# Optimization experiments

Hardware: AMD Instinct MI355X
Metric: run time of the kernel (lower is better)

The kernel has to match this reference:

```python
import jax, jax.numpy as jnp
import numpy as np

N = 32768       # flattened residues (batch*seq)
DIM = 1024      # dim == channel (required by residual add)
NRES = 21       # amino-acid types
RECYCLES = 2


def _quat_to_rot(q):
    w, x, y, z = q[..., 0], q[..., 1], q[..., 2], q[..., 3]
    return jnp.stack([
        jnp.stack([1 - 2 * (y * y + z * z), 2 * (x * y - w * z), 2 * (x * z + w * y)], -1),
        jnp.stack([2 * (x * y + w * z), 1 - 2 * (x * x + z * z), 2 * (y * z - w * x)], -1),
        jnp.stack([2 * (x * z - w * y), 2 * (y * z + w * x), 1 - 2 * (x * x + y * y)], -1),
    ], -2)


def _rand_rigid(key, shape, tscale=1.0):
    # random valid rigid transforms as 4x4 homogeneous matrices
    kq, kt = jax.random.split(key)
    q = jax.random.normal(kq, shape + (4,), jnp.float32)
    q = q / jnp.linalg.norm(q, axis=-1, keepdims=True)
    rot = _quat_to_rot(q)
    t = jax.random.normal(kt, shape + (3,), jnp.float32) * tscale
    m = jnp.zeros(shape + (4, 4), jnp.float32)
    m = m.at[..., :3, :3].set(rot).at[..., :3, 3].set(t).at[..., 3, 3].set(1.0)
    return m


def setup_inputs():
    key = jax.random.key(0)
    ks = jax.random.split(key, 12)
    s = 1.0 / np.sqrt(DIM)
    return {
        "rep0": jax.random.normal(ks[0], (N, DIM), jnp.float32),
        "rep1": jax.random.normal(ks[1], (N, DIM), jnp.float32),
        "w_in": jax.random.normal(ks[2], (DIM, DIM), jnp.float32) * s,
        "b_in": jnp.zeros((DIM,), jnp.float32),
        "w1": jax.random.normal(ks[3], (DIM, DIM), jnp.float32) * s,
        "b1": jnp.zeros((DIM,), jnp.float32),
        "w2": jax.random.normal(ks[4], (DIM, DIM), jnp.float32) * s,
        "b2": jnp.zeros((DIM,), jnp.float32),
        "w_ang": jax.random.normal(ks[5], (DIM, 14), jnp.float32) * s,
        "b_ang": jnp.zeros((14,), jnp.float32),
        "rigids": _rand_rigid(ks[6], (N,), tscale=10.0),              # backbone frames
        "default_frames": _rand_rigid(ks[7], (NRES, 8), tscale=1.5), # restype_rigid_group_default_frame
        "lit_positions": jax.random.normal(ks[8], (NRES, 14, 3), jnp.float32),
        "atom_mask": (jax.random.uniform(ks[9], (NRES, 14)) > 0.2).astype(jnp.float32),
        "aatype": jax.random.randint(ks[10], (N,), 0, NRES),
        "group_idx": jax.random.randint(ks[11], (NRES, 14), 0, 8),   # restype_atom14_to_rigid_group
    }


def reference(rep0, rep1, w_in, b_in, w1, b1, w2, b2, w_ang, b_ang,
              rigids, default_frames, lit_positions, atom_mask, aatype, group_idx):
    # InputProjection: shared ReLU+Linear applied to each representation, summed
    act = (jax.nn.relu(rep0) @ w_in + b_in) + (jax.nn.relu(rep1) @ w_in + b_in)
    # ResidueBlock with residual recycles: act += Linear(ReLU(Linear(ReLU(act))))
    for _ in range(RECYCLES):
        h = jax.nn.relu(act) @ w1 + b1
        h = jax.nn.relu(h) @ w2 + b2
        act = act + h
    # TorisonAngles: Linear(dim,14) -> (N,7,2) -> l2_normalize
    ang = (jax.nn.relu(act) @ w_ang + b_ang).reshape(N, 7, 2)
    angles = ang / jnp.sqrt(jnp.maximum(jnp.sum(ang * ang, -1, keepdims=True), 1e-12))
    # torsion_angles_to_frames: prepend identity backbone angle (sin=0, cos=1)
    sin = jnp.concatenate([jnp.zeros((N, 1), angles.dtype), angles[..., 0]], 1)  # [N,8]
    cos = jnp.concatenate([jnp.ones((N, 1), angles.dtype), angles[..., 1]], 1)
    z = jnp.zeros_like(sin); one = jnp.ones_like(sin)
    rotx = jnp.stack([
        jnp.stack([one, z, z, z], -1),
        jnp.stack([z, cos, -sin, z], -1),
        jnp.stack([z, sin, cos, z], -1),
        jnp.stack([z, z, z, one], -1),
    ], -2)                                            # [N,8,4,4] rotation about x by torsion
    frames = default_frames[aatype] @ rotx            # [N,8,4,4]
    # chi2/chi3/chi4 frames are defined relative to the previous chi frame
    f5 = frames[:, 4] @ frames[:, 5]
    f6 = f5 @ frames[:, 6]
    f7 = f6 @ frames[:, 7]
    frames_to_bb = jnp.concatenate([frames[:, :5], jnp.stack([f5, f6, f7], 1)], 1)
    frames_global = rigids[:, None] @ frames_to_bb    # [N,8,4,4]
    # frames_and_literature_positions_to_atom14_pos
    gidx = group_idx[aatype]                          # [N,14] rigid-group id per atom
    f14 = jnp.take_along_axis(frames_global,
                              jnp.broadcast_to(gidx[:, :, None, None], (N, 14, 4, 4)),
                              axis=1)                 # [N,14,4,4]
    pos = lit_positions[aatype]                       # [N,14,3]
    pred = jnp.einsum('naij,naj->nai', f14[..., :3, :3], pos) + f14[..., :3, 3]
    pred = pred * atom_mask[aatype][..., None]        # [N,14,3]
    return angles, pred, frames_global
```

## Files before the change

### kernel.cpp

```cpp
#include <hip/hip_runtime.h>
#include <stdint.h>

typedef uint16_t u16;
typedef uint32_t u32;
typedef __bf16 bf16;
typedef bf16 bf16x8 __attribute__((ext_vector_type(8)));
typedef float f32x4 __attribute__((ext_vector_type(4)));

#define N_RES 32768
#define DIM 1024

__device__ __forceinline__ float b2f(u16 u) {
  u32 v = ((u32)u) << 16;
  float f;
  __builtin_memcpy(&f, &v, 4);
  return f;
}
__device__ __forceinline__ u16 f2b(float f) {
  u32 u;
  __builtin_memcpy(&u, &f, 4);
  u += 0x7fffu + ((u >> 16) & 1u);
  return (u16)(u >> 16);
}
__device__ __forceinline__ void split2(float v, u16& h, u16& l) {
  h = f2b(v);
  l = f2b(v - b2f(h));
}
__device__ __forceinline__ void relu_mask4(uint4& h, uint4& l) {
  u32 s, m;
  s = h.x & 0x80008000u; m = ((s >> 15) & 0x00010001u) * 0xFFFFu; h.x &= ~m; l.x &= ~m;
  s = h.y & 0x80008000u; m = ((s >> 15) & 0x00010001u) * 0xFFFFu; h.y &= ~m; l.y &= ~m;
  s = h.z & 0x80008000u; m = ((s >> 15) & 0x00010001u) * 0xFFFFu; h.z &= ~m; l.z &= ~m;
  s = h.w & 0x80008000u; m = ((s >> 15) & 0x00010001u) * 0xFFFFu; h.w &= ~m; l.w &= ~m;
}
__device__ __forceinline__ void relu_split8(bf16x8& h, bf16x8& l) {
  uint4 uh, ul;
  __builtin_memcpy(&uh, &h, 16);
  __builtin_memcpy(&ul, &l, 16);
  relu_mask4(uh, ul);
  __builtin_memcpy(&h, &uh, 16);
  __builtin_memcpy(&l, &ul, 16);
}
__device__ __forceinline__ void split8(const float* v, uint4& H, uint4& L) {
  u16 h[8], l[8];
#pragma unroll
  for (int i = 0; i < 8; ++i) split2(v[i], h[i], l[i]);
  H.x = (u32)h[0] | ((u32)h[1] << 16);
  H.y = (u32)h[2] | ((u32)h[3] << 16);
  H.z = (u32)h[4] | ((u32)h[5] << 16);
  H.w = (u32)h[6] | ((u32)h[7] << 16);
  L.x = (u32)l[0] | ((u32)l[1] << 16);
  L.y = (u32)l[2] | ((u32)l[3] << 16);
  L.z = (u32)l[4] | ((u32)l[5] << 16);
  L.w = (u32)l[6] | ((u32)l[7] << 16);
}

__device__ __forceinline__ void g2l16(const void* g, void* lds) {
  __builtin_amdgcn_global_load_lds(
      (__attribute__((address_space(1))) void*)(g),
      (__attribute__((address_space(3))) void*)(lds), 16, 0, 0);
}

__global__ __launch_bounds__(256) void transpose_split(const float* __restrict__ in,
                                                       u16* __restrict__ outh,
                                                       u16* __restrict__ outl) {
  __shared__ float t[32][33];
  const int bx = blockIdx.x * 32, by = blockIdx.y * 32;
  const int tx = threadIdx.x, ty = threadIdx.y;
  for (int i = ty; i < 32; i += 8) t[i][tx] = in[(size_t)(by + i) * DIM + bx + tx];
  __syncthreads();
  for (int i = ty; i < 32; i += 8) {
    u16 h, l;
    split2(t[tx][i], h, l);
    const size_t o = (size_t)(bx + i) * DIM + by + tx;
    outh[o] = h;
    outl[o] = l;
  }
}

__global__ __launch_bounds__(256) void prep_input(const float* __restrict__ rep0,
                                                  const float* __restrict__ rep1,
                                                  u16* __restrict__ oh,
                                                  u16* __restrict__ ol) {
  const size_t base = ((size_t)blockIdx.x * 256 + threadIdx.x) * 8;
  float4 x0 = *(const float4*)(rep0 + base);
  float4 x1 = *(const float4*)(rep0 + base + 4);
  float4 y0 = *(const float4*)(rep1 + base);
  float4 y1 = *(const float4*)(rep1 + base + 4);
  float v[8];
  v[0] = fmaxf(x0.x, 0.f) + fmaxf(y0.x, 0.f);
  v[1] = fmaxf(x0.y, 0.f) + fmaxf(y0.y, 0.f);
  v[2] = fmaxf(x0.z, 0.f) + fmaxf(y0.z, 0.f);
  v[3] = fmaxf(x0.w, 0.f) + fmaxf(y0.w, 0.f);
  v[4] = fmaxf(x1.x, 0.f) + fmaxf(y1.x, 0.f);
  v[5] = fmaxf(x1.y, 0.f) + fmaxf(y1.y, 0.f);
  v[6] = fmaxf(x1.z, 0.f) + fmaxf(y1.z, 0.f);
  v[7] = fmaxf(x1.w, 0.f) + fmaxf(y1.w, 0.f);
  uint4 H, L;
  split8(v, H, L);
  *(uint4*)(oh + base) = H;
  *(uint4*)(ol + base) = L;
}

__global__ __launch_bounds__(256, 3) void gemm_split(
    const u16* __restrict__ Ah, const u16* __restrict__ Al, int reluA,
    const u16* __restrict__ Bh, const u16* __restrict__ Bl,
    const float* __restrict__ bias, float bscale,
    const u16* __restrict__ Rh, const u16* __restrict__ Rl,
    u16* __restrict__ Oh, u16* __restrict__ Ol) {
  __shared__ __align__(16) u32 SMEM[6144];
  u16* AS = (u16*)SMEM;
  u16* BS = (u16*)SMEM + 8192;
  u32* C_lds = SMEM;

  const int tid = threadIdx.x;
  const int wave = tid >> 6;
  const int lane = tid & 63;
  const int lrow = lane & 15;
  const int lquad = lane >> 4;

  const int g = blockIdx.x + (blockIdx.y << 4);
  const int xcd = g & 7;
  const int j = g >> 3;
  const int bm = (xcd * 32 + (j >> 4)) * 128;
  const int bn = (j & 15) * 64;

  const int wm = (wave & 1) * 64;
  const int wn = (wave >> 1) * 32;

  f32x4 acc[4][2];
#pragma unroll
  for (int i = 0; i < 4; ++i)
#pragma unroll
    for (int jj = 0; jj < 2; ++jj) acc[i][jj] = (f32x4){0.f, 0.f, 0.f, 0.f};

  const int srow = tid >> 3;
  const int dc = (tid & 7) ^ (srow & 7);
  const size_t scol = (size_t)(dc & 3) * 8;
  const u16* srcA = ((dc < 4) ? Ah : Al) + (size_t)(bm + srow) * DIM + scol;
  const u16* srcB = ((dc < 4) ? Bh : Bl) + (size_t)(bn + srow) * DIM + scol;
  u16* dA = AS + (size_t)tid * 8;
  u16* dB = BS + (size_t)tid * 8;

  const int swzH = ((lquad ^ (lrow & 7)) * 8);
  const int swzL = swzH ^ 32;

  for (int kt = 0; kt < 32; ++kt) {
    const size_t ko = (size_t)kt * 32;
#pragma unroll
    for (int is = 0; is < 4; ++is)
      g2l16(srcA + ko + (size_t)is * 32 * DIM, dA + is * 2048);
#pragma unroll
    for (int is = 0; is < 2; ++is)
      g2l16(srcB + ko + (size_t)is * 32 * DIM, dB + is * 2048);
    __syncthreads();

    bf16x8 a_h[4], a_l[4], b_h[2], b_l[2];
#pragma unroll
    for (int i = 0; i < 4; ++i) {
      const u16* arow = AS + (wm + i * 16 + lrow) * 64;
      a_h[i] = *(const bf16x8*)(arow + swzH);
      a_l[i] = *(const bf16x8*)(arow + swzL);
      if (reluA) relu_split8(a_h[i], a_l[i]);
    }
#pragma unroll
    for (int jj = 0; jj < 2; ++jj) {
      const u16* brow = BS + (wn + jj * 16 + lrow) * 64;
      b_h[jj] = *(const bf16x8*)(brow + swzH);
      b_l[jj] = *(const bf16x8*)(brow + swzL);
    }
#pragma unroll
    for (int i = 0; i < 4; ++i)
#pragma unroll
      for (int jj = 0; jj < 2; ++jj) {
        acc[i][jj] = __builtin_amdgcn_mfma_f32_16x16x32_bf16(a_h[i], b_h[jj], acc[i][jj], 0, 0, 0);
        acc[i][jj] = __builtin_amdgcn_mfma_f32_16x16x32_bf16(a_h[i], b_l[jj], acc[i][jj], 0, 0, 0);
        acc[i][jj] = __builtin_amdgcn_mfma_f32_16x16x32_bf16(a_l[i], b_h[jj], acc[i][jj], 0, 0, 0);
      }
    __syncthreads();
  }

#pragma unroll
  for (int half = 0; half < 2; ++half) {
    if (wm == half * 64) {
#pragma unroll
      for (int jj = 0; jj < 2; ++jj) {
        const int colL = wn + jj * 16 + lrow;
        const float bj = bias[bn + colL] * bscale;
#pragma unroll
        for (int i = 0; i < 4; ++i) {
#pragma unroll
          for (int r = 0; r < 4; ++r) {
            const int row = i * 16 + lquad * 4 + r;
            u16 h, l;
            split2(acc[i][jj][r] + bj, h, l);
            C_lds[row * 64 + (colL ^ ((row & 7) << 2))] = (u32)h | ((u32)l << 16);
          }
        }
      }
    }
    __syncthreads();
    {
      const int wv = tid >> 6;
      const int lr8 = (lane >> 3);
      const int cg = lane & 7;
#pragma unroll
      for (int g2 = 0; g2 < 2; ++g2) {
        const int row = wv * 16 + g2 * 8 + lr8;
        const int swz = (row & 7) << 2;
        const u32* crow = C_lds + row * 64;
        const int cb = cg * 8;
        uint4 qa = *(const uint4*)&crow[cb ^ swz];
        uint4 qb = *(const uint4*)&crow[(cb + 4) ^ swz];
        float v[8];
        v[0] = b2f((u16)(qa.x & 0xFFFF)) + b2f((u16)(qa.x >> 16));
        v[1] = b2f((u16)(qa.y & 0xFFFF)) + b2f((u16)(qa.y >> 16));
        v[2] = b2f((u16)(qa.z & 0xFFFF)) + b2f((u16)(qa.z >> 16));
        v[3] = b2f((u16)(qa.w & 0xFFFF)) + b2f((u16)(qa.w >> 16));
        v[4] = b2f((u16)(qb.x & 0xFFFF)) + b2f((u16)(qb.x >> 16));
        v[5] = b2f((u16)(qb.y & 0xFFFF)) + b2f((u16)(qb.y >> 16));
        v[6] = b2f((u16)(qb.z & 0xFFFF)) + b2f((u16)(qb.z >> 16));
        v[7] = b2f((u16)(qb.w & 0xFFFF)) + b2f((u16)(qb.w >> 16));
        const int grow = bm + half * 64 + row;
        const size_t gbase = (size_t)grow * DIM + bn + cb;
        if (Rh) {
          uint4 rh = *(const uint4*)(Rh + gbase);
          uint4 rl = *(const uint4*)(Rl + gbase);
          v[0] += b2f((u16)(rh.x & 0xFFFF)) + b2f((u16)(rl.x & 0xFFFF));
          v[1] += b2f((u16)(rh.x >> 16)) + b2f((u16)(rl.x >> 16));
          v[2] += b2f((u16)(rh.y & 0xFFFF)) + b2f((u16)(rl.y & 0xFFFF));
          v[3] += b2f((u16)(rh.y >> 16)) + b2f((u16)(rl.y >> 16));
          v[4] += b2f((u16)(rh.z & 0xFFFF)) + b2f((u16)(rl.z & 0xFFFF));
          v[5] += b2f((u16)(rh.z >> 16)) + b2f((u16)(rl.z >> 16));
          v[6] += b2f((u16)(rh.w & 0xFFFF)) + b2f((u16)(rl.w & 0xFFFF));
          v[7] += b2f((u16)(rh.w >> 16)) + b2f((u16)(rl.w >> 16));
        }
        uint4 H, L;
        split8(v, H, L);
        *(uint4*)(Oh + gbase) = H;
        *(uint4*)(Ol + gbase) = L;
      }
    }
    __syncthreads();
  }
}

__global__ __launch_bounds__(256) void angles_split(
    const u16* __restrict__ ACTh, const u16* __restrict__ ACTl,
    const u16* __restrict__ WAh, const u16* __restrict__ WAl,
    const float* __restrict__ b_ang, float* __restrict__ out_angles) {
  const int tid = threadIdx.x;
  const int wave = tid >> 6, lane = tid & 63;
  const int lrow = lane & 15, lquad = lane >> 4;
  const int rowA = blockIdx.x * 64 + wave * 16 + lrow;
  f32x4 acc = (f32x4){0.f, 0.f, 0.f, 0.f};
  const u16* gah = ACTh + (size_t)rowA * DIM + lquad * 8;
  const u16* gal = ACTl + (size_t)rowA * DIM + lquad * 8;
  const u16* gbh = WAh + (size_t)lrow * DIM + lquad * 8;
  const u16* gbl = WAl + (size_t)lrow * DIM + lquad * 8;
#pragma unroll 4
  for (int kb = 0; kb < DIM; kb += 32) {
    bf16x8 ah = *(const bf16x8*)(gah + kb);
    bf16x8 al = *(const bf16x8*)(gal + kb);
    relu_split8(ah, al);
    bf16x8 bh = *(const bf16x8*)(gbh + kb);
    bf16x8 bl = *(const bf16x8*)(gbl + kb);
    acc = __builtin_amdgcn_mfma_f32_16x16x32_bf16(ah, bh, acc, 0, 0, 0);
    acc = __builtin_amdgcn_mfma_f32_16x16x32_bf16(ah, bl, acc, 0, 0, 0);
    acc = __builtin_amdgcn_mfma_f32_16x16x32_bf16(al, bh, acc, 0, 0, 0);
  }
  const int col = lrow;
  const float bj = (col < 14) ? b_ang[col] : 0.f;
#pragma unroll
  for (int r = 0; r < 4; ++r) {
    float v = acc[r] + bj;
    float p = __shfl_xor(v, 1, 64);
    float s2 = fmaxf(v * v + p * p, 1e-12f);
    float o = v * rsqrtf(s2);
    const int orow = blockIdx.x * 64 + wave * 16 + lquad * 4 + r;
    if (col < 14) out_angles[(size_t)orow * 14 + col] = o;
  }
}

__global__ __launch_bounds__(256) void prep_wang(const float* __restrict__ w,
                                                 u16* __restrict__ outh,
                                                 u16* __restrict__ outl) {
  for (int idx = threadIdx.x; idx < 16 * 1024; idx += 256) {
    const int n = idx & 15;
    const int k = idx >> 4;
    const float v = (n < 14) ? w[(size_t)k * 14 + n] : 0.f;
    u16 h, l;
    split2(v, h, l);
    outh[(size_t)n * DIM + k] = h;
    outl[(size_t)n * DIM + k] = l;
  }
}

__device__ __forceinline__ void mm34(const float* A, const float* B, float* O) {
#pragma unroll
  for (int r = 0; r < 3; ++r) {
#pragma unroll
    for (int c = 0; c < 4; ++c) {
      float v = A[r * 4 + 0] * B[0 * 4 + c] + A[r * 4 + 1] * B[1 * 4 + c] +
                A[r * 4 + 2] * B[2 * 4 + c];
      if (c == 3) v += A[r * 4 + 3];
      O[r * 4 + c] = v;
    }
  }
}

__global__ __launch_bounds__(256) void frames_kernel(
    const float* __restrict__ angles, const float* __restrict__ rigids,
    const float* __restrict__ dframes, const float* __restrict__ litpos,
    const float* __restrict__ amask, const int* __restrict__ aatype,
    const int* __restrict__ gidx, float* __restrict__ out_pred,
    float* __restrict__ out_frames) {
  const int n = blockIdx.x * 256 + threadIdx.x;
  const int aa = aatype[n];

  float fr[8][12];
  const float* angp = angles + (size_t)n * 14;
#pragma unroll
  for (int g = 0; g < 8; ++g) {
    float s, c;
    if (g == 0) { s = 0.f; c = 1.f; }
    else { s = angp[(g - 1) * 2]; c = angp[(g - 1) * 2 + 1]; }
    const float* D = dframes + ((size_t)aa * 8 + g) * 16;
#pragma unroll
    for (int r = 0; r < 3; ++r) {
      float d0 = D[r * 4 + 0], d1 = D[r * 4 + 1], d2 = D[r * 4 + 2], d3 = D[r * 4 + 3];
      fr[g][r * 4 + 0] = d0;
      fr[g][r * 4 + 1] = d1 * c + d2 * s;
      fr[g][r * 4 + 2] = d2 * c - d1 * s;
      fr[g][r * 4 + 3] = d3;
    }
  }
  float tmp[12];
  mm34(fr[4], fr[5], tmp);
#pragma unroll
  for (int e = 0; e < 12; ++e) fr[5][e] = tmp[e];
  mm34(fr[5], fr[6], tmp);
#pragma unroll
  for (int e = 0; e < 12; ++e) fr[6][e] = tmp[e];
  mm34(fr[6], fr[7], tmp);
#pragma unroll
  for (int e = 0; e < 12; ++e) fr[7][e] = tmp[e];

  float R[12];
  const float* rp = rigids + (size_t)n * 16;
#pragma unroll
  for (int e = 0; e < 12; ++e) R[e] = rp[e];
#pragma unroll
  for (int g = 0; g < 8; ++g) {
    mm34(R, fr[g], tmp);
#pragma unroll
    for (int e = 0; e < 12; ++e) fr[g][e] = tmp[e];
  }

  float4* of = (float4*)(out_frames + (size_t)n * 128);
#pragma unroll
  for (int g = 0; g < 8; ++g) {
    of[g * 4 + 0] = (float4){fr[g][0], fr[g][1], fr[g][2], fr[g][3]};
    of[g * 4 + 1] = (float4){fr[g][4], fr[g][5], fr[g][6], fr[g][7]};
    of[g * 4 + 2] = (float4){fr[g][8], fr[g][9], fr[g][10], fr[g][11]};
    of[g * 4 + 3] = (float4){0.f, 0.f, 0.f, 1.f};
  }

  float P[42];
#pragma unroll
  for (int a = 0; a < 14; ++a) {
    const int g = gidx[aa * 14 + a];
    float f[12];
#pragma unroll
    for (int q = 0; q < 8; ++q) {
      if (q == 0) {
#pragma unroll
        for (int e = 0; e < 12; ++e) f[e] = fr[0][e];
      } else {
        const bool sel = (g == q);
#pragma unroll
        for (int e = 0; e < 12; ++e) f[e] = sel ? fr[q][e] : f[e];
      }
    }
    const float px = litpos[((size_t)aa * 14 + a) * 3 + 0];
    const float py = litpos[((size_t)aa * 14 + a) * 3 + 1];
    const float pz = litpos[((size_t)aa * 14 + a) * 3 + 2];
    const float mk = amask[aa * 14 + a];
    P[a * 3 + 0] = (f[0] * px + f[1] * py + f[2] * pz + f[3]) * mk;
    P[a * 3 + 1] = (f[4] * px + f[5] * py + f[6] * pz + f[7]) * mk;
    P[a * 3 + 2] = (f[8] * px + f[9] * py + f[10] * pz + f[11]) * mk;
  }
  float2* op = (float2*)(out_pred + (size_t)n * 42);
#pragma unroll
  for (int i = 0; i < 21; ++i) op[i] = (float2){P[2 * i], P[2 * i + 1]};
}

__global__ __launch_bounds__(256) void ws_diag(float* __restrict__ out, float mb) {
  const int i = blockIdx.x * 256 + threadIdx.x;
  if (i < N_RES * 14) out[i] = mb;
}

extern "C" void kernel_launch(void* const* d_in, const int* in_sizes, int n_in,
                              void* d_out, int out_size, void* d_ws, size_t ws_size,
                              hipStream_t stream) {
  const float* rep0 = (const float*)d_in[0];
  const float* rep1 = (const float*)d_in[1];
  const float* w_in = (const float*)d_in[2];
  const float* b_in = (const float*)d_in[3];
  const float* w1 = (const float*)d_in[4];
  const float* b1 = (const float*)d_in[5];
  const float* w2 = (const float*)d_in[6];
  const float* b2 = (const float*)d_in[7];
  const float* w_ang = (const float*)d_in[8];
  const float* b_ang = (const float*)d_in[9];
  const float* rigids = (const float*)d_in[10];
  const float* dframes = (const float*)d_in[11];
  const float* litpos = (const float*)d_in[12];
  const float* amask = (const float*)d_in[13];
  const int* aatype = (const int*)d_in[14];
  const int* gidx = (const int*)d_in[15];

  const size_t SLOT = (size_t)N_RES * DIM;
  const size_t NEED_U16 = 4 * SLOT + 6 * (size_t)DIM * DIM + 2 * 16 * DIM;

  float* out_ang = (float*)d_out;
  float* out_pred = out_ang + (size_t)N_RES * 14;
  float* out_frames = out_pred + (size_t)N_RES * 42;

  if (ws_size < NEED_U16 * 2) {
    ws_diag<<<(N_RES * 14 + 255) / 256, 256, 0, stream>>>(
        out_ang, (float)(ws_size >> 20));
    return;
  }

  u16* ACTh = (u16*)d_ws;
  u16* ACTl = ACTh + SLOT;
  u16* Hh = ACTl + SLOT;
  u16* Hl = Hh + SLOT;
  u16* W0h = Hl + SLOT;
  u16* W0l = W0h + (size_t)DIM * DIM;
  u16* W1h = W0l + (size_t)DIM * DIM;
  u16* W1l = W1h + (size_t)DIM * DIM;
  u16* W2h = W1l + (size_t)DIM * DIM;
  u16* W2l = W2h + (size_t)DIM * DIM;
  u16* WAh = W2l + (size_t)DIM * DIM;
  u16* WAl = WAh + (size_t)16 * DIM;

  transpose_split<<<dim3(32, 32), dim3(32, 8), 0, stream>>>(w_in, W0h, W0l);
  transpose_split<<<dim3(32, 32), dim3(32, 8), 0, stream>>>(w1, W1h, W1l);
  transpose_split<<<dim3(32, 32), dim3(32, 8), 0, stream>>>(w2, W2h, W2l);
  prep_wang<<<1, 256, 0, stream>>>(w_ang, WAh, WAl);

  prep_input<<<(N_RES * DIM / 8) / 256, 256, 0, stream>>>(rep0, rep1, Hh, Hl);

  dim3 gg(DIM / 64, N_RES / 128);
  gemm_split<<<gg, 256, 0, stream>>>(Hh, Hl, 0, W0h, W0l, b_in, 2.f,
                                     nullptr, nullptr, ACTh, ACTl);
  gemm_split<<<gg, 256, 0, stream>>>(ACTh, ACTl, 1, W1h, W1l, b1, 1.f,
                                     nullptr, nullptr, Hh, Hl);
  gemm_split<<<gg, 256, 0, stream>>>(Hh, Hl, 1, W2h, W2l, b2, 1.f,
                                     ACTh, ACTl, ACTh, ACTl);
  gemm_split<<<gg, 256, 0, stream>>>(ACTh, ACTl, 1, W1h, W1l, b1, 1.f,
                                     nullptr, nullptr, Hh, Hl);
  gemm_split<<<gg, 256, 0, stream>>>(Hh, Hl, 1, W2h, W2l, b2, 1.f,
                                     ACTh, ACTl, ACTh, ACTl);

  angles_split<<<N_RES / 64, 256, 0, stream>>>(ACTh, ACTl, WAh, WAl, b_ang,
                                               out_ang);
  frames_kernel<<<N_RES / 256, 256, 0, stream>>>(out_ang, rigids, dframes, litpos,
                                                 amask, aatype, gidx, out_pred,
                                                 out_frames);
}
```

Baseline: 1.729 ms.

## Double-buffer GEMM LDS tiles and move ReLU into the GEMM epilogue

The split-bf16 GEMM now uses two LDS buffers, so the global-to-LDS load of the next K tile is issued before computing the current one. Synchronisation uses explicit vmcnt waits and raw barriers to hide load latency. ReLU on the hidden activations moves from the A-operand load path (done every K step) to the output epilogue of the producing GEMM, and the final residual output is ReLU'd so the angles kernel can skip it. This doubles LDS use per block, which may lower occupancy, and it relies on the hand-written waitcnt count being correct.

```diff
diff --git a/kernel.cpp b/kernel.cpp
--- a/kernel.cpp
+++ b/kernel.cpp
@@ -105,12 +105,11 @@
 __global__ __launch_bounds__(256, 3) void gemm_split(
     const u16* __restrict__ Ah, const u16* __restrict__ Al, int reluA,
     const u16* __restrict__ Bh, const u16* __restrict__ Bl,
-    const float* __restrict__ bias, float bscale,
+    const float* __restrict__ bias, float bscale, int reluOut,
     const u16* __restrict__ Rh, const u16* __restrict__ Rl,
     u16* __restrict__ Oh, u16* __restrict__ Ol) {
-  __shared__ __align__(16) u32 SMEM[6144];
-  u16* AS = (u16*)SMEM;
-  u16* BS = (u16*)SMEM + 8192;
+  __shared__ __align__(16) u32 SMEM[12288];
+  u16* SM = (u16*)SMEM;
   u32* C_lds = SMEM;
 
   const int tid = threadIdx.x;
@@ -139,33 +138,39 @@
   const size_t scol = (size_t)(dc & 3) * 8;
   const u16* srcA = ((dc < 4) ? Ah : Al) + (size_t)(bm + srow) * DIM + scol;
   const u16* srcB = ((dc < 4) ? Bh : Bl) + (size_t)(bn + srow) * DIM + scol;
-  u16* dA = AS + (size_t)tid * 8;
-  u16* dB = BS + (size_t)tid * 8;
+  u16* wA0 = SM + (size_t)tid * 8;
+  u16* wB0 = SM + 8192 + (size_t)tid * 8;
+  u16* wA1 = SM + 12288 + (size_t)tid * 8;
+  u16* wB1 = SM + 20480 + (size_t)tid * 8;
+  const u16* rA0 = SM;
+  const u16* rB0 = SM + 8192;
+  const u16* rA1 = SM + 12288;
+  const u16* rB1 = SM + 20480;
 
   const int swzH = ((lquad ^ (lrow & 7)) * 8);
   const int swzL = swzH ^ 32;
 
-  for (int kt = 0; kt < 32; ++kt) {
+  auto stage = [&](u16* dA, u16* dB, int kt) {
     const size_t ko = (size_t)kt * 32;
-#pragma unroll
-    for (int is = 0; is < 4; ++is)
-      g2l16(srcA + ko + (size_t)is * 32 * DIM, dA + is * 2048);
-#pragma unroll
-    for (int is = 0; is < 2; ++is)
-      g2l16(srcB + ko + (size_t)is * 32 * DIM, dB + is * 2048);
-    __syncthreads();
-
+    g2l16(srcA + ko, dA);
+    g2l16(srcA + ko + (size_t)32 * DIM, dA + 2048);
+    g2l16(srcA + ko + (size_t)64 * DIM, dA + 4096);
+    g2l16(srcA + ko + (size_t)96 * DIM, dA + 6144);
+    g2l16(srcB + ko, dB);
+    g2l16(srcB + ko + (size_t)32 * DIM, dB + 2048);
+  };
+  auto compute = [&](const u16* rA, const u16* rB) {
     bf16x8 a_h[4], a_l[4], b_h[2], b_l[2];
 #pragma unroll
     for (int i = 0; i < 4; ++i) {
-      const u16* arow = AS + (wm + i * 16 + lrow) * 64;
+      const u16* arow = rA + (wm + i * 16 + lrow) * 64;
       a_h[i] = *(const bf16x8*)(arow + swzH);
       a_l[i] = *(const bf16x8*)(arow + swzL);
       if (reluA) relu_split8(a_h[i], a_l[i]);
     }
 #pragma unroll
     for (int jj = 0; jj < 2; ++jj) {
-      const u16* brow = BS + (wn + jj * 16 + lrow) * 64;
+      const u16* brow = rB + (wn + jj * 16 + lrow) * 64;
       b_h[jj] = *(const bf16x8*)(brow + swzH);
       b_l[jj] = *(const bf16x8*)(brow + swzL);
     }
@@ -177,8 +182,22 @@
         acc[i][jj] = __builtin_amdgcn_mfma_f32_16x16x32_bf16(a_h[i], b_l[jj], acc[i][jj], 0, 0, 0);
         acc[i][jj] = __builtin_amdgcn_mfma_f32_16x16x32_bf16(a_l[i], b_h[jj], acc[i][jj], 0, 0, 0);
       }
-    __syncthreads();
-  }
+  };
+
+  stage(wA0, wB0, 0);
+  for (int kt = 0; kt < 32; kt += 2) {
+    stage(wA1, wB1, kt + 1);
+    asm volatile("s_waitcnt vmcnt(6)" ::: "memory");
+    asm volatile("s_barrier" ::: "memory");
+    compute(rA0, rB0);
+    asm volatile("s_barrier" ::: "memory");
+    stage(wA0, wB0, (kt + 2 < 32) ? kt + 2 : 31);
+    asm volatile("s_waitcnt vmcnt(6)" ::: "memory");
+    asm volatile("s_barrier" ::: "memory");
+    compute(rA1, rB1);
+    asm volatile("s_barrier" ::: "memory");
+  }
+  __syncthreads();
 
 #pragma unroll
   for (int half = 0; half < 2; ++half) {
@@ -235,6 +254,10 @@
           v[6] += b2f((u16)(rh.w & 0xFFFF)) + b2f((u16)(rl.w & 0xFFFF));
           v[7] += b2f((u16)(rh.w >> 16)) + b2f((u16)(rl.w >> 16));
         }
+        if (reluOut) {
+#pragma unroll
+          for (int e = 0; e < 8; ++e) v[e] = fmaxf(v[e], 0.f);
+        }
         uint4 H, L;
         split8(v, H, L);
         *(uint4*)(Oh + gbase) = H;
@@ -262,7 +285,6 @@
   for (int kb = 0; kb < DIM; kb += 32) {
     bf16x8 ah = *(const bf16x8*)(gah + kb);
     bf16x8 al = *(const bf16x8*)(gal + kb);
-    relu_split8(ah, al);
     bf16x8 bh = *(const bf16x8*)(gbh + kb);
     bf16x8 bl = *(const bf16x8*)(gbl + kb);
     acc = __builtin_amdgcn_mfma_f32_16x16x32_bf16(ah, bh, acc, 0, 0, 0);
@@ -454,15 +476,15 @@
   prep_input<<<(N_RES * DIM / 8) / 256, 256, 0, stream>>>(rep0, rep1, Hh, Hl);
 
   dim3 gg(DIM / 64, N_RES / 128);
-  gemm_split<<<gg, 256, 0, stream>>>(Hh, Hl, 0, W0h, W0l, b_in, 2.f,
+  gemm_split<<<gg, 256, 0, stream>>>(Hh, Hl, 0, W0h, W0l, b_in, 2.f, 0,
                                      nullptr, nullptr, ACTh, ACTl);
-  gemm_split<<<gg, 256, 0, stream>>>(ACTh, ACTl, 1, W1h, W1l, b1, 1.f,
+  gemm_split<<<gg, 256, 0, stream>>>(ACTh, ACTl, 1, W1h, W1l, b1, 1.f, 1,
                                      nullptr, nullptr, Hh, Hl);
-  gemm_split<<<gg, 256, 0, stream>>>(Hh, Hl, 1, W2h, W2l, b2, 1.f,
+  gemm_split<<<gg, 256, 0, stream>>>(Hh, Hl, 0, W2h, W2l, b2, 1.f, 0,
                                      ACTh, ACTl, ACTh, ACTl);
-  gemm_split<<<gg, 256, 0, stream>>>(ACTh, ACTl, 1, W1h, W1l, b1, 1.f,
+  gemm_split<<<gg, 256, 0, stream>>>(ACTh, ACTl, 1, W1h, W1l, b1, 1.f, 1,
                                      nullptr, nullptr, Hh, Hl);
-  gemm_split<<<gg, 256, 0, stream>>>(Hh, Hl, 1, W2h, W2l, b2, 1.f,
+  gemm_split<<<gg, 256, 0, stream>>>(Hh, Hl, 0, W2h, W2l, b2, 1.f, 1,
                                      ACTh, ACTl, ACTh, ACTl);
 
   angles_split<<<N_RES / 64, 256, 0, stream>>>(ACTh, ACTl, WAh, WAl, b_ang,
```

Measured after the change: 1.673 ms. 3.2% less time.
